# Kernel optimization log

Hardware: AMD Instinct MI355X
Metric: run time of the kernel (lower is better)

The kernel has to match this reference:

```python
import jax, jax.numpy as jnp
import numpy as np

HEADS = 12
DIM_HEAD = 64
INNER = HEADS * DIM_HEAD  # 768
DIM = 512
KS = 3


def setup_inputs() -> dict:
    key = jax.random.key(0)
    ks = jax.random.split(key, 5)
    B, H, W = 8, 32, 32
    N = H * W + 1  # +1 cls token -> has_cls path
    x = jax.random.normal(ks[0], (B, N, DIM), dtype=jnp.float32)
    w_qkv = jax.random.normal(ks[1], (3 * INNER, DIM), dtype=jnp.float32) * (DIM ** -0.5)
    w_dw = jax.random.normal(ks[2], (DIM, 1, KS, KS), dtype=jnp.float32) * (1.0 / KS)
    w_out = jax.random.normal(ks[3], (DIM, INNER), dtype=jnp.float32) * (INNER ** -0.5)
    b_out = jax.random.normal(ks[4], (DIM,), dtype=jnp.float32) * 0.01
    return {"x": x, "w_qkv": w_qkv, "w_dw": w_dw, "w_out": w_out,
            "b_out": b_out, "h_feat": H, "w_feat": W}


def reference(x, w_qkv, w_dw, w_out, b_out, h_feat, w_feat):
    B, N, C = x.shape
    scale = DIM_HEAD ** -0.5
    # qkv projection (Linear, no bias): torch weight layout (out,in)
    qkv = jnp.einsum('bnc,oc->bno', x, w_qkv)  # (B,N,3*INNER)
    q, k, v = jnp.split(qkv, 3, axis=-1)

    def split_heads(t):
        return t.reshape(B, N, HEADS, DIM_HEAD).transpose(0, 2, 1, 3)  # (B,H,N,d)

    q, k, v = map(split_heads, (q, k, v))
    dots = jnp.einsum('bhid,bhjd->bhij', q, k) * scale
    attn = jax.nn.softmax(dots, axis=-1)
    out_attn = jnp.einsum('bhij,bhjd->bhid', attn, v)
    out_attn = out_attn.transpose(0, 2, 1, 3).reshape(B, N, INNER)

    has_cls = (N == h_feat * w_feat + 1)  # static
    spatial = x[:, 1:, :] if has_cls else x
    spatial_2d = spatial.transpose(0, 2, 1).reshape(B, C, h_feat, w_feat)
    # depthwise conv, padding = ks//2 (SAME for odd ks, stride 1)
    loc = jax.lax.conv_general_dilated(
        spatial_2d, w_dw, window_strides=(1, 1), padding='SAME',
        feature_group_count=C,
        dimension_numbers=('NCHW', 'OIHW', 'NCHW'))
    local_out = loc.reshape(B, C, h_feat * w_feat).transpose(0, 2, 1)  # (B,hw,C)
    if has_cls:
        cls_out = x[:, :1, :INNER]  # C < INNER so this is the full cls token
        local_out = jnp.concatenate([cls_out, local_out], axis=1)  # (B,N,C)
    if local_out.shape[-1] < INNER:
        out = out_attn + jnp.pad(
            local_out, ((0, 0), (0, 0), (0, INNER - local_out.shape[-1])))
    else:
        out = out_attn
    # output Linear (dropout=0 in eval)
    return jnp.einsum('bni,oi->bno', out, w_out) + b_out
```

## Files before the change

### kernel.cpp

```cpp
#include <hip/hip_runtime.h>
#include <hip/hip_bf16.h>
#include <stdint.h>
#include <math.h>

typedef __bf16 bf16;
typedef __bf16 bf16x8 __attribute__((ext_vector_type(8)));
typedef float f32x4 __attribute__((ext_vector_type(4)));
typedef short s4 __attribute__((ext_vector_type(4)));

#define QSCALE 0.1803368801111f


__device__ __forceinline__ void gload_lds16(const void* g, void* l) {
  typedef const __attribute__((address_space(1))) char g_char;
  typedef __attribute__((address_space(3))) char l_char;
  g_char* gp = (g_char*)(uintptr_t)g;
  l_char* lp = (l_char*)(uint32_t)(uintptr_t)l;
  __builtin_amdgcn_global_load_lds(gp, lp, 16, 0, 0);
}

__device__ __forceinline__ float fexp2(float x) {
#if __has_builtin(__builtin_amdgcn_exp2f)
  return __builtin_amdgcn_exp2f(x);
#else
  return exp2f(x);
#endif
}

__device__ __forceinline__ float frcp(float x) {
#if __has_builtin(__builtin_amdgcn_rcpf)
  return __builtin_amdgcn_rcpf(x);
#else
  return 1.f / x;
#endif
}

__device__ __forceinline__ uint32_t pk2(float a, float b) {
  union { bf16 h; unsigned short u; } ua, ub;
  ua.h = (bf16)a; ub.h = (bf16)b;
  return (uint32_t)ua.u | ((uint32_t)ub.u << 16);
}

__device__ __forceinline__ f32x4 pv_mfma(s4 a, s4 b, f32x4 c) {
#if __has_builtin(__builtin_amdgcn_mfma_f32_16x16x16bf16_1k)
  return __builtin_amdgcn_mfma_f32_16x16x16bf16_1k(a, b, c, 0, 0, 0);
#else
  asm volatile("v_mfma_f32_16x16x16_bf16 %0, %1, %2, %0" : "+v"(c) : "v"(a), "v"(b));
  return c;
#endif
}

__global__ __launch_bounds__(256) void k_prep(const float* __restrict__ x,
                                              const float* __restrict__ wqkv,
                                              const float* __restrict__ wout,
                                              bf16* __restrict__ xb, bf16* __restrict__ wqkvb,
                                              bf16* __restrict__ woutb,
                                              const float* __restrict__ wdw,
                                              bf16* __restrict__ locb) {
  if (blockIdx.x >= 2848) {
    const int lb = blockIdx.x - 2848;
    const int b = lb >> 8;
    const int y = (lb >> 3) & 31;
    const int xseg = lb & 7;
    const int c = threadIdx.x * 2;
    const int x0 = xseg * 4;
    const bool hm = (y > 0), hp = (y < 31);
    float wa[9], wb[9];
#pragma unroll
    for (int k = 0; k < 9; ++k) {
      wa[k] = wdw[(size_t)c * 9 + k];
      wb[k] = wdw[(size_t)(c + 1) * 9 + k];
    }
    const float* xrow = x + ((size_t)b * 1025 + 1) * 512 + c;
    float A0 = 0.f, B0 = 0.f, A1 = 0.f, B1 = 0.f;
    for (int cc = x0 - 1; cc <= x0 + 4; ++cc) {
      float2 v0 = make_float2(0.f, 0.f), v1 = v0, v2 = v0;
      if (cc >= 0 && cc < 32) {
        v1 = *(const float2*)&xrow[((size_t)y * 32 + cc) * 512];
        if (hm) v0 = *(const float2*)&xrow[((size_t)(y - 1) * 32 + cc) * 512];
        if (hp) v2 = *(const float2*)&xrow[((size_t)(y + 1) * 32 + cc) * 512];
      }
      float t0a = v0.x * wa[0] + v1.x * wa[3] + v2.x * wa[6];
      float t1a = v0.x * wa[1] + v1.x * wa[4] + v2.x * wa[7];
      float t2a = v0.x * wa[2] + v1.x * wa[5] + v2.x * wa[8];
      float t0b = v0.y * wb[0] + v1.y * wb[3] + v2.y * wb[6];
      float t1b = v0.y * wb[1] + v1.y * wb[4] + v2.y * wb[7];
      float t2b = v0.y * wb[2] + v1.y * wb[5] + v2.y * wb[8];
      int oc = cc - 1;
      if (oc >= x0 && oc <= x0 + 3) {
        size_t o = ((size_t)b * 1025 + 1 + y * 32 + oc) * 512 + c;
        *(uint32_t*)&locb[o] = pk2(A0 + t2a, A1 + t2b);
      }
      A0 = B0 + t1a; B0 = t0a;
      A1 = B1 + t1b; B1 = t0b;
    }
    if (y == 0 && xseg == 0) {
      float2 xc = *(const float2*)&x[((size_t)b * 1025) * 512 + c];
      *(uint32_t*)&locb[((size_t)b * 1025) * 512 + c] = pk2(xc.x, xc.y);
    }
    return;
  }
  int u = blockIdx.x * 256 + threadIdx.x;
  const float* src = nullptr;
  bf16* dst = nullptr;
  bool zero = false;
  if (u < 532480) {
    if (u >= 524800) zero = true;
    src = x; dst = xb;
  } else if (u < 679936) {
    u -= 532480; src = wqkv; dst = wqkvb;
  } else {
    u -= 679936; src = wout; dst = woutb;
  }
  float4 a = make_float4(0.f, 0.f, 0.f, 0.f), bq = a;
  if (!zero) {
    a  = *(const float4*)&src[(size_t)u * 8];
    bq = *(const float4*)&src[(size_t)u * 8 + 4];
  }
  uint4 p;
  p.x = pk2(a.x, a.y);
  p.y = pk2(a.z, a.w);
  p.z = pk2(bq.x, bq.y);
  p.w = pk2(bq.z, bq.w);
  *(uint4*)&dst[(size_t)u * 8] = p;
}

template <int EPI, int BM, int BN, int NTN, int TPB>
__global__ __launch_bounds__(TPB) void k_gemm(const bf16* __restrict__ A,
                                              const bf16* __restrict__ Bt, int K,
                                              bf16* __restrict__ q, bf16* __restrict__ kk,
                                              bf16* __restrict__ vt,
                                              const float* __restrict__ bias,
                                              float* __restrict__ out) {
  __shared__ __attribute__((aligned(16))) bf16 smem[3 * (BM + BN) * 32];
  constexpr int NWAVE = TPB / 64;
  constexpr int WCN = (NWAVE == 8) ? 4 : 2;
  constexpr int WRN = NWAVE / WCN;
  constexpr int WROWS = BM / WRN, WCOLS = BN / WCN;
  constexpr int MF = WROWS / 16, NF = WCOLS / 16;
  constexpr int AL = BM / 16 / NWAVE;
  constexpr int BL = BN / 16 / NWAVE;
  constexpr int LOADS = AL + BL;
  const int tid = threadIdx.x;
  const int lane = tid & 63;
  const int w = tid >> 6;
  const int wr = w / WCN, wc = w % WCN;
  const int l15 = lane & 15, l4 = lane >> 4;

  auto sAb = [&](int bi) { return smem + bi * (BM * 32); };
  auto sBb = [&](int bi) { return smem + 3 * BM * 32 + bi * (BN * 32); };

  const int nwg = gridDim.x;
  const int qq = nwg >> 3, rr = nwg & 7;
  const int xcd = blockIdx.x & 7, idx = blockIdx.x >> 3;
  const int logical = (xcd < rr) ? xcd * (qq + 1) + idx
                                 : rr * (qq + 1) + (xcd - rr) * qq + idx;
  const int tm = logical / NTN, tn = logical - tm * NTN;

  f32x4 acc[MF][NF] = {};

  const int srow = lane >> 2, schunk = lane & 3;
  const int rA = w * (AL * 16) + srow;
  const bf16* aS = A + ((size_t)(tm * BM + rA)) * K + ((schunk ^ ((rA >> 1) & 3)) * 8);
  const int rB = w * (BL * 16) + srow;
  const bf16* bS = Bt + ((size_t)(tn * BN + rB)) * K + ((schunk ^ ((rB >> 1) & 3)) * 8);

  auto STAGE = [&](int bi, int kt) {
    size_t o = (size_t)kt * 32;
#pragma unroll
    for (int i = 0; i < AL; ++i)
      gload_lds16(aS + (size_t)i * 16 * K + o, &sAb(bi)[(w * (AL * 16) + i * 16) * 32]);
#pragma unroll
    for (int i = 0; i < BL; ++i)
      gload_lds16(bS + (size_t)i * 16 * K + o, &sBb(bi)[(w * (BL * 16) + i * 16) * 32]);
  };

  STAGE(0, 0);
  STAGE(1, 1);
  int cur = 0;
  const int Ksteps = K >> 5;
  for (int kt = 0; kt < Ksteps; ++kt) {
    if (kt + 1 < Ksteps) {
      if constexpr (LOADS == 4)      asm volatile("s_waitcnt vmcnt(4)" ::: "memory");
      else if constexpr (LOADS == 3) asm volatile("s_waitcnt vmcnt(3)" ::: "memory");
      else                           asm volatile("s_waitcnt vmcnt(2)" ::: "memory");
    } else {
      asm volatile("s_waitcnt vmcnt(0)" ::: "memory");
    }
    __builtin_amdgcn_s_barrier();
    __builtin_amdgcn_sched_barrier(0);
    if (kt + 2 < Ksteps) {
      int b2 = cur + 2; if (b2 >= 3) b2 -= 3;
      STAGE(b2, kt + 2);
    }

    const bf16* a_ = sAb(cur);
    const bf16* b_ = sBb(cur);
    bf16x8 af[MF], bfr[NF];
#pragma unroll
    for (int mf = 0; mf < MF; ++mf) {
      int row = wr * WROWS + mf * 16 + l15;
      int phys = l4 ^ ((row >> 1) & 3);
      af[mf] = *(const bf16x8*)&a_[row * 32 + phys * 8];
    }
#pragma unroll
    for (int nf = 0; nf < NF; ++nf) {
      int row = wc * WCOLS + nf * 16 + l15;
      int phys = l4 ^ ((row >> 1) & 3);
      bfr[nf] = *(const bf16x8*)&b_[row * 32 + phys * 8];
    }
    __builtin_amdgcn_s_setprio(1);
#pragma unroll
    for (int mf = 0; mf < MF; ++mf)
#pragma unroll
      for (int nf = 0; nf < NF; ++nf)
        acc[mf][nf] =
            __builtin_amdgcn_mfma_f32_16x16x32_bf16(bfr[nf], af[mf], acc[mf][nf], 0, 0, 0);
    __builtin_amdgcn_s_setprio(0);
    ++cur; if (cur >= 3) cur = 0;
  }

  const int RbaseL = tm * BM + wr * WROWS + l15;
  const int CbaseL = tn * BN + wc * WCOLS + l4 * 4;

  if (EPI == 0 && tn < 12) {
    constexpr int PAD = 132;
    const int seg = tn / 6;
    const float scl = seg ? 1.f : QSCALE;
    bf16* ct = smem;
    __syncthreads();
#pragma unroll
    for (int mf = 0; mf < MF; ++mf) {
      int rl = wr * WROWS + mf * 16 + l15;
#pragma unroll
      for (int nf = 0; nf < NF; ++nf) {
        int cl = wc * WCOLS + nf * 16 + l4 * 4;
        uint2 p;
        p.x = pk2(acc[mf][nf][0] * scl, acc[mf][nf][1] * scl);
        p.y = pk2(acc[mf][nf][2] * scl, acc[mf][nf][3] * scl);
        *(uint2*)&ct[rl * PAD + cl] = p;
      }
    }
    __syncthreads();
    bf16* dst = seg ? kk : q;
    const int h0 = tn * 2 - seg * 12;
#pragma unroll
    for (int it = 0; it < BM * 32 / TPB; ++it) {
      int u = it * TPB + tid;
      int row = u >> 5;
      int R = tm * BM + row;
      if (R >= 8200) continue;
      int b = R / 1025, n = R - b * 1025;
      int hh = (u >> 4) & 1;
      int d0 = (u & 15) * 4;
      uint2 v = *(const uint2*)&ct[row * PAD + hh * 64 + d0];
      *(uint2*)&dst[(((size_t)b * 12 + h0 + hh) * 1088 + n) * 64 + d0] = v;
    }
    return;
  }

#pragma unroll
  for (int mf = 0; mf < MF; ++mf) {
    int R = RbaseL + mf * 16;
    if (R >= 8200) continue;
    if (EPI == 0) {
      int b = R / 1025;
      int n = R - b * 1025;
      int kvq = n >> 2, e = n & 3;
#pragma unroll
      for (int nf = 0; nf < NF; ++nf) {
        int Cc0 = CbaseL + nf * 16;
        int inner = Cc0 - 1536;
        int h = inner >> 6, d0 = inner & 63;
        bf16* vb = &vt[(((size_t)(b * 12 + h) * 272 + kvq) * 64 + d0) * 4 + e];
#pragma unroll
        for (int r = 0; r < 4; ++r) vb[r * 4] = (bf16)acc[mf][nf][r];
      }
    } else {
#pragma unroll
      for (int nf = 0; nf < NF; ++nf) {
        int Cc0 = CbaseL + nf * 16;
        float4 bz = *(const float4*)&bias[Cc0];
        float4 o4;
        o4.x = acc[mf][nf][0] + bz.x;
        o4.y = acc[mf][nf][1] + bz.y;
        o4.z = acc[mf][nf][2] + bz.z;
        o4.w = acc[mf][nf][3] + bz.w;
        *(float4*)&out[(size_t)R * 512 + Cc0] = o4;
      }
    }
  }
}

__global__ __launch_bounds__(512) void k_flash(const bf16* __restrict__ qg,
                                               const bf16* __restrict__ kg,
                                               const bf16* __restrict__ vpg,
                                               const bf16* __restrict__ locb,
                                               bf16* __restrict__ outb) {
  __shared__ __attribute__((aligned(16))) bf16 sK[2][64 * 64];
  __shared__ __attribute__((aligned(16))) bf16 sVP[2][16 * 256];
  const int tid = threadIdx.x, lane = tid & 63, w = tid >> 6;
  const int l15 = lane & 15, l4 = lane >> 4;
  const int wg = blockIdx.x;
  const int logical = (wg & 7) * 108 + (wg >> 3);
  const int bh = logical / 9, qgp = logical - bh * 9;
  const int b = bh / 12, h = bh - b * 12;

  size_t qoff = ((size_t)bh * 1088 + qgp * 128 + w * 16 + l15) * 64 + l4 * 8;
  const bf16x8 qf0 = *(const bf16x8*)&qg[qoff];
  const bf16x8 qf1 = *(const bf16x8*)&qg[qoff + 32];

  float lreg = 0.f;
  f32x4 oa[4] = {};

  const int px0 = (l4 ^ (l15 & 7)) * 8;
  const int px1 = ((4 + l4) ^ (l15 & 7)) * 8;

  const int rowK = w * 8 + (lane >> 3);
  const int clogK = (lane & 7) ^ (rowK & 7);
  const bf16* kS = kg + ((size_t)bh * 1088 + rowK) * 64 + clogK * 8;
  const bf16* vS = vpg + (size_t)bh * 69632 + w * 512 + lane * 8;
  const int kD = w * 512;
  const int vD = w * 512;

  auto STAGE = [&](int bi, int t) {
    size_t o = (size_t)t * 4096;
    gload_lds16(kS + o, &sK[bi][kD]);
    gload_lds16(vS + o, &sVP[bi][vD]);
  };

  STAGE(0, 0);
  int cur = 0;

  for (int t = 0; t < 16; ++t) {
    asm volatile("s_waitcnt vmcnt(0)" ::: "memory");
    __builtin_amdgcn_s_barrier();
    __builtin_amdgcn_sched_barrier(0);
    if (t < 15) STAGE(cur ^ 1, t + 1);

    const bf16* kb_ = sK[cur];
    const bf16* vpb = sVP[cur];

    f32x4 sc[4] = {};
    __builtin_amdgcn_s_setprio(1);
#pragma unroll
    for (int jt = 0; jt < 4; ++jt) {
      bf16x8 a0 = *(const bf16x8*)&kb_[(jt * 16 + l15) * 64 + px0];
      sc[jt] = __builtin_amdgcn_mfma_f32_16x16x32_bf16(a0, qf0, sc[jt], 0, 0, 0);
    }
#pragma unroll
    for (int jt = 0; jt < 4; ++jt) {
      bf16x8 a1 = *(const bf16x8*)&kb_[(jt * 16 + l15) * 64 + px1];
      sc[jt] = __builtin_amdgcn_mfma_f32_16x16x32_bf16(a1, qf1, sc[jt], 0, 0, 0);
    }
    __builtin_amdgcn_s_setprio(0);

    union { uint32_t u[2]; s4 v; } pa[4];
    float lsum = 0.f;
#pragma unroll
    for (int jt = 0; jt < 4; ++jt) {
      float p0 = fexp2(sc[jt][0]);
      float p1 = fexp2(sc[jt][1]);
      float p2 = fexp2(sc[jt][2]);
      float p3 = fexp2(sc[jt][3]);
      lsum += (p0 + p1) + (p2 + p3);
      pa[jt].u[0] = pk2(p0, p1);
      pa[jt].u[1] = pk2(p2, p3);
    }
    lreg += lsum;

    __builtin_amdgcn_s_setprio(1);
#pragma unroll
    for (int jt = 0; jt < 4; ++jt)
#pragma unroll
      for (int db = 0; db < 4; ++db) {
        s4 vf = *(const s4*)&vpb[((jt * 4 + l4) * 64 + db * 16 + l15) * 4];
        oa[db] = pv_mfma(pa[jt].v, vf, oa[db]);
      }
    __builtin_amdgcn_s_setprio(0);
    cur ^= 1;
  }

  {
    const bf16* k1 = kg + ((size_t)bh * 1088 + 1024) * 64;
    bf16x8 kA = *(const bf16x8*)&k1[l4 * 8];
    bf16x8 kB = *(const bf16x8*)&k1[32 + l4 * 8];
    float s = 0.f;
#pragma unroll
    for (int e = 0; e < 8; ++e)
      s += (float)qf0[e] * (float)kA[e] + (float)qf1[e] * (float)kB[e];
    s += __shfl_xor(s, 16);
    s += __shfl_xor(s, 32);
    float p = fexp2(s);
    if (l4 == 0) lreg += p;
    float pr[4];
#pragma unroll
    for (int r = 0; r < 4; ++r) pr[r] = __shfl(p, l4 * 4 + r);
    const bf16* v1 = vpg + (size_t)bh * 69632 + 65536;
#pragma unroll
    for (int db = 0; db < 4; ++db) {
      float vd = (float)v1[(db * 16 + l15) * 4];
#pragma unroll
      for (int r = 0; r < 4; ++r) oa[db][r] += pr[r] * vd;
    }
  }

  float ls = lreg;
  ls += __shfl_xor(ls, 16);
  ls += __shfl_xor(ls, 32);
  float linv = frcp(ls);
#pragma unroll
  for (int r = 0; r < 4; ++r) {
    float ir = __shfl(linv, l4 * 4 + r);
    int n = qgp * 128 + w * 16 + l4 * 4 + r;
    if (n >= 1025) continue;
#pragma unroll
    for (int db = 0; db < 4; ++db) {
      float v = oa[db][r] * ir;
      if (h < 8)
        v += (float)locb[((size_t)b * 1025 + n) * 512 + h * 64 + db * 16 + l15];
      outb[((size_t)b * 1025 + n) * 768 + h * 64 + db * 16 + l15] = (bf16)v;
    }
  }
}

extern "C" void kernel_launch(void* const* d_in, const int* in_sizes, int n_in,
                              void* d_out, int out_size, void* d_ws, size_t ws_size,
                              hipStream_t stream) {
  const float* x = (const float*)d_in[0];
  const float* w_qkv = (const float*)d_in[1];
  const float* w_dw = (const float*)d_in[2];
  const float* w_out = (const float*)d_in[3];
  const float* b_out = (const float*)d_in[4];
  float* out = (float*)d_out;

  char* ws = (char*)d_ws;
  size_t off = 0;
  auto alloc = [&](size_t bytes) {
    char* p = ws + off;
    off = (off + bytes + 255) & ~(size_t)255;
    return p;
  };
  bf16* xb    = (bf16*)alloc((size_t)8320 * 512 * 2);
  bf16* wqkvb = (bf16*)alloc((size_t)2304 * 512 * 2);
  bf16* woutb = (bf16*)alloc((size_t)512 * 768 * 2);
  bf16* qb    = (bf16*)alloc((size_t)96 * 1088 * 64 * 2);
  bf16* kb    = (bf16*)alloc((size_t)96 * 1088 * 64 * 2);
  bf16* vP    = (bf16*)alloc((size_t)96 * 272 * 64 * 4 * 2);
  bf16* locb  = (bf16*)alloc((size_t)8 * 1025 * 512 * 2);
  bf16* outb  = (bf16*)alloc((size_t)8320 * 768 * 2);

  k_prep<<<4896, 256, 0, stream>>>(x, w_qkv, w_out, xb, wqkvb, woutb, w_dw, locb);
  k_gemm<0, 128, 128, 18, 512><<<1170, 512, 0, stream>>>(xb, wqkvb, 512, qb, kb, vP,
                                                         nullptr, nullptr);
  k_flash<<<864, 512, 0, stream>>>(qb, kb, vP, locb, outb);
  k_gemm<1, 128, 64, 8, 256><<<520, 256, 0, stream>>>(outb, woutb, 768, nullptr, nullptr,
                                                      nullptr, b_out, out);
}
```

Before: 128.6 us.

## Tile depthwise conv over 4x4 patches and run output GEMM with 512 threads

The depthwise-conv blocks in the prep kernel now each cover a 4x4 spatial patch instead of a 1x4 row segment. Six input rows are loaded per column and reused across four output rows, which cuts redundant global reads and the block count. The output-projection GEMM moves from 256 to 512 threads per block. Because the B tile now has fewer 16-row blocks than waves, only some waves load B, with per-wave waitcnt values to match. More waves give better latency hiding for that GEMM but make the load split uneven.

```diff
diff --git a/kernel.cpp b/kernel.cpp
--- a/kernel.cpp
+++ b/kernel.cpp
@@ -59,12 +59,11 @@
                                               bf16* __restrict__ locb) {
   if (blockIdx.x >= 2848) {
     const int lb = blockIdx.x - 2848;
-    const int b = lb >> 8;
-    const int y = (lb >> 3) & 31;
+    const int b = lb >> 6;
+    const int yseg = (lb >> 3) & 7;
     const int xseg = lb & 7;
     const int c = threadIdx.x * 2;
-    const int x0 = xseg * 4;
-    const bool hm = (y > 0), hp = (y < 31);
+    const int x0 = xseg * 4, y0 = yseg * 4;
     float wa[9], wb[9];
 #pragma unroll
     for (int k = 0; k < 9; ++k) {
@@ -72,29 +71,36 @@
       wb[k] = wdw[(size_t)(c + 1) * 9 + k];
     }
     const float* xrow = x + ((size_t)b * 1025 + 1) * 512 + c;
-    float A0 = 0.f, B0 = 0.f, A1 = 0.f, B1 = 0.f;
+    float A0[4] = {}, B0[4] = {}, A1[4] = {}, B1[4] = {};
     for (int cc = x0 - 1; cc <= x0 + 4; ++cc) {
-      float2 v0 = make_float2(0.f, 0.f), v1 = v0, v2 = v0;
-      if (cc >= 0 && cc < 32) {
-        v1 = *(const float2*)&xrow[((size_t)y * 32 + cc) * 512];
-        if (hm) v0 = *(const float2*)&xrow[((size_t)(y - 1) * 32 + cc) * 512];
-        if (hp) v2 = *(const float2*)&xrow[((size_t)(y + 1) * 32 + cc) * 512];
-      }
-      float t0a = v0.x * wa[0] + v1.x * wa[3] + v2.x * wa[6];
-      float t1a = v0.x * wa[1] + v1.x * wa[4] + v2.x * wa[7];
-      float t2a = v0.x * wa[2] + v1.x * wa[5] + v2.x * wa[8];
-      float t0b = v0.y * wb[0] + v1.y * wb[3] + v2.y * wb[6];
-      float t1b = v0.y * wb[1] + v1.y * wb[4] + v2.y * wb[7];
-      float t2b = v0.y * wb[2] + v1.y * wb[5] + v2.y * wb[8];
+      const bool cok = (cc >= 0 && cc < 32);
+      float2 v[6];
+#pragma unroll
+      for (int i = 0; i < 6; ++i) {
+        int ry = y0 - 1 + i;
+        v[i] = (cok && ry >= 0 && ry <= 31)
+                   ? *(const float2*)&xrow[((size_t)ry * 32 + cc) * 512]
+                   : make_float2(0.f, 0.f);
+      }
       int oc = cc - 1;
-      if (oc >= x0 && oc <= x0 + 3) {
-        size_t o = ((size_t)b * 1025 + 1 + y * 32 + oc) * 512 + c;
-        *(uint32_t*)&locb[o] = pk2(A0 + t2a, A1 + t2b);
-      }
-      A0 = B0 + t1a; B0 = t0a;
-      A1 = B1 + t1b; B1 = t0b;
-    }
-    if (y == 0 && xseg == 0) {
+      bool wok = (oc >= x0 && oc <= x0 + 3);
+#pragma unroll
+      for (int j = 0; j < 4; ++j) {
+        float t0a = v[j].x * wa[0] + v[j + 1].x * wa[3] + v[j + 2].x * wa[6];
+        float t1a = v[j].x * wa[1] + v[j + 1].x * wa[4] + v[j + 2].x * wa[7];
+        float t2a = v[j].x * wa[2] + v[j + 1].x * wa[5] + v[j + 2].x * wa[8];
+        float t0b = v[j].y * wb[0] + v[j + 1].y * wb[3] + v[j + 2].y * wb[6];
+        float t1b = v[j].y * wb[1] + v[j + 1].y * wb[4] + v[j + 2].y * wb[7];
+        float t2b = v[j].y * wb[2] + v[j + 1].y * wb[5] + v[j + 2].y * wb[8];
+        if (wok) {
+          size_t o = ((size_t)b * 1025 + 1 + (y0 + j) * 32 + oc) * 512 + c;
+          *(uint32_t*)&locb[o] = pk2(A0[j] + t2a, A1[j] + t2b);
+        }
+        A0[j] = B0[j] + t1a; B0[j] = t0a;
+        A1[j] = B1[j] + t1b; B1[j] = t0b;
+      }
+    }
+    if (yseg == 0 && xseg == 0) {
       float2 xc = *(const float2*)&x[((size_t)b * 1025) * 512 + c];
       *(uint32_t*)&locb[((size_t)b * 1025) * 512 + c] = pk2(xc.x, xc.y);
     }
@@ -139,8 +145,9 @@
   constexpr int WROWS = BM / WRN, WCOLS = BN / WCN;
   constexpr int MF = WROWS / 16, NF = WCOLS / 16;
   constexpr int AL = BM / 16 / NWAVE;
-  constexpr int BL = BN / 16 / NWAVE;
-  constexpr int LOADS = AL + BL;
+  constexpr int BBLK = BN / 16;
+  constexpr bool BSPLIT = (BBLK < NWAVE);
+  constexpr int BL = BSPLIT ? 1 : (BBLK / NWAVE);
   const int tid = threadIdx.x;
   const int lane = tid & 63;
   const int w = tid >> 6;
@@ -162,7 +169,7 @@
   const int srow = lane >> 2, schunk = lane & 3;
   const int rA = w * (AL * 16) + srow;
   const bf16* aS = A + ((size_t)(tm * BM + rA)) * K + ((schunk ^ ((rA >> 1) & 3)) * 8);
-  const int rB = w * (BL * 16) + srow;
+  const int rB = (BSPLIT ? w * 16 : w * (BL * 16)) + srow;
   const bf16* bS = Bt + ((size_t)(tn * BN + rB)) * K + ((schunk ^ ((rB >> 1) & 3)) * 8);
 
   auto STAGE = [&](int bi, int kt) {
@@ -170,9 +177,13 @@
 #pragma unroll
     for (int i = 0; i < AL; ++i)
       gload_lds16(aS + (size_t)i * 16 * K + o, &sAb(bi)[(w * (AL * 16) + i * 16) * 32]);
-#pragma unroll
-    for (int i = 0; i < BL; ++i)
-      gload_lds16(bS + (size_t)i * 16 * K + o, &sBb(bi)[(w * (BL * 16) + i * 16) * 32]);
+    if constexpr (BSPLIT) {
+      if (w < BBLK) gload_lds16(bS + o, &sBb(bi)[(w * 16) * 32]);
+    } else {
+#pragma unroll
+      for (int i = 0; i < BL; ++i)
+        gload_lds16(bS + (size_t)i * 16 * K + o, &sBb(bi)[(w * (BL * 16) + i * 16) * 32]);
+    }
   };
 
   STAGE(0, 0);
@@ -181,9 +192,15 @@
   const int Ksteps = K >> 5;
   for (int kt = 0; kt < Ksteps; ++kt) {
     if (kt + 1 < Ksteps) {
-      if constexpr (LOADS == 4)      asm volatile("s_waitcnt vmcnt(4)" ::: "memory");
-      else if constexpr (LOADS == 3) asm volatile("s_waitcnt vmcnt(3)" ::: "memory");
-      else                           asm volatile("s_waitcnt vmcnt(2)" ::: "memory");
+      if constexpr (BSPLIT) {
+        if (w < BBLK) asm volatile("s_waitcnt vmcnt(2)" ::: "memory");
+        else          asm volatile("s_waitcnt vmcnt(1)" ::: "memory");
+      } else {
+        constexpr int LOADS = AL + BL;
+        if constexpr (LOADS == 4)      asm volatile("s_waitcnt vmcnt(4)" ::: "memory");
+        else if constexpr (LOADS == 3) asm volatile("s_waitcnt vmcnt(3)" ::: "memory");
+        else                           asm volatile("s_waitcnt vmcnt(2)" ::: "memory");
+      }
     } else {
       asm volatile("s_waitcnt vmcnt(0)" ::: "memory");
     }
@@ -450,10 +467,10 @@
   bf16* locb  = (bf16*)alloc((size_t)8 * 1025 * 512 * 2);
   bf16* outb  = (bf16*)alloc((size_t)8320 * 768 * 2);
 
-  k_prep<<<4896, 256, 0, stream>>>(x, w_qkv, w_out, xb, wqkvb, woutb, w_dw, locb);
+  k_prep<<<3360, 256, 0, stream>>>(x, w_qkv, w_out, xb, wqkvb, woutb, w_dw, locb);
   k_gemm<0, 128, 128, 18, 512><<<1170, 512, 0, stream>>>(xb, wqkvb, 512, qb, kb, vP,
                                                          nullptr, nullptr);
   k_flash<<<864, 512, 0, stream>>>(qb, kb, vP, locb, outb);
-  k_gemm<1, 128, 64, 8, 256><<<520, 256, 0, stream>>>(outb, woutb, 768, nullptr, nullptr,
+  k_gemm<1, 128, 64, 8, 512><<<520, 512, 0, stream>>>(outb, woutb, 768, nullptr, nullptr,
                                                       nullptr, b_out, out);
 }
```

New measurement: 130.0 us. About the same (+1.1%).
